# Kernel tuning notes

Hardware: AMD Instinct MI355X
Metric: run time of the kernel (lower is better)

Reference implementation:

```python
import jax, jax.numpy as jnp
import numpy as np

B, N, P = 64, 800000, 128          # batch, total CpG features, n_pathways (capsules)
H1, H2, C = 256, 128, 32           # MLP hidden_topology and n_output
EPS = 1e-5                         # BatchNorm1d eps


def _xavier(key, fan_in, fan_out, shape):
    bound = np.sqrt(6.0 / (fan_in + fan_out))
    return jax.random.uniform(key, shape, jnp.float32, -bound, bound)


def setup_inputs() -> dict:
    key = jax.random.key(0)
    ks = jax.random.split(key, 10)
    x = jax.random.normal(ks[0], (B, N), jnp.float32)
    # idx: sorted pathway assignment, equal capsule sizes N//P (matches module_lens)
    idx = jnp.sort(jax.random.randint(ks[1], (N,), 0, P)).astype(jnp.int64)
    # SPWModulesLayer.weight: xavier_uniform on shape (1, N)
    w = _xavier(ks[2], N, 1, (N,))
    co_w = jax.random.uniform(ks[3], (P,), jnp.float32, 0.0, 4.0)  # CancelOut init
    bn0_g, bn0_b = jnp.ones(P, jnp.float32), jnp.zeros(P, jnp.float32)
    W1, b1 = _xavier(ks[4], P, H1, (P, H1)), jnp.zeros(H1, jnp.float32)
    bn1_g, bn1_b = jnp.ones(H1, jnp.float32), jnp.zeros(H1, jnp.float32)
    W2, b2 = _xavier(ks[5], H1, H2, (H1, H2)), jnp.zeros(H2, jnp.float32)
    bn2_g, bn2_b = jnp.ones(H2, jnp.float32), jnp.zeros(H2, jnp.float32)
    Wo, bo = _xavier(ks[6], H2, C, (H2, C)), jnp.zeros(C, jnp.float32)
    return {"x": x, "w": w, "co_w": co_w,
            "bn0_g": bn0_g, "bn0_b": bn0_b,
            "W1": W1, "b1": b1, "bn1_g": bn1_g, "bn1_b": bn1_b,
            "W2": W2, "b2": b2, "bn2_g": bn2_g, "bn2_b": bn2_b,
            "Wo": Wo, "bo": bo, "idx": idx}


def _bn(z, g, b):
    # BatchNorm1d in training mode: batch mean, biased variance
    m = jnp.mean(z, axis=0)
    v = jnp.mean((z - m) ** 2, axis=0)
    return (z - m) * jax.lax.rsqrt(v + EPS) * g + b


def reference(x, w, co_w, bn0_g, bn0_b, W1, b1, bn1_g, bn1_b,
              W2, b2, bn2_g, bn2_b, Wo, bo, idx):
    # --- SPWModulesLayer: weighted scatter_add over pathway index (last dim) ---
    WX = jnp.zeros((x.shape[0], P), x.dtype).at[:, idx].add(x * w)   # [B, P]
    Z = _bn(jax.nn.relu(WX), bn0_g, bn0_b)                           # ReLU + BN
    Z = Z * jax.nn.sigmoid(co_w)                                     # CancelOut
    # --- MLP head: Linear->ReLU->BN twice, then Linear->Softmax ---
    h = _bn(jax.nn.relu(Z @ W1 + b1), bn1_g, bn1_b)
    h = _bn(jax.nn.relu(h @ W2 + b2), bn2_g, bn2_b)
    y = jax.nn.softmax(h @ Wo + bo, axis=-1)
    return (y, Z)
```

## Files before the change

kernel.cpp:

```cpp
#include <hip/hip_runtime.h>
#include <hip/hip_bf16.h>

#define BB     64
#define NF4    200000
#define NSEG   782
#define NP     128
#define NH1    256
#define NH2    128
#define NC     32
#define EPSV   1e-5f

typedef float fx4 __attribute__((ext_vector_type(4)));

__device__ __forceinline__ float dot4(fx4 a, fx4 b) {
    return fmaf(a[0], b[0], fmaf(a[1], b[1], fmaf(a[2], b[2], a[3] * b[3])));
}

__global__ __launch_bounds__(256) void k_scatter(
    const float* __restrict__ x, const float* __restrict__ w,
    const int* __restrict__ idx, float* __restrict__ WX)
{
    const int blk = blockIdx.x;
    const int b   = blk & 31;
    const int seg = blk >> 5;
    const int tid = threadIdx.x;
    const int n4  = seg * 256 + tid;
    const int waveBase = seg * 256 + (tid & ~63);
    if (waveBase + 63 >= NF4) {
        if (waveBase >= NF4) return;
    }
    if (n4 >= NF4) return;
    const int lane = tid & 63;

    const int  pLo = idx[waveBase * 4];
    const int  pHi = idx[waveBase * 4 + 255];
    const bool uniform = (pLo == pHi);

    const fx4  wv = reinterpret_cast<const fx4*>(w)[n4];
    const int4 pv = reinterpret_cast<const int4*>(idx)[n4];
    const fx4  xA = reinterpret_cast<const fx4*>(x)[(size_t)b * NF4 + n4];
    const fx4  xB = reinterpret_cast<const fx4*>(x)[(size_t)(b + 32) * NF4 + n4];

    fx4 wLo;
    wLo[0] = (pv.x == pLo) ? wv[0] : 0.f;
    wLo[1] = (pv.y == pLo) ? wv[1] : 0.f;
    wLo[2] = (pv.z == pLo) ? wv[2] : 0.f;
    wLo[3] = (pv.w == pLo) ? wv[3] : 0.f;

    float aLo = dot4(xA, wLo);
    float bLo = dot4(xB, wLo);
    #pragma unroll
    for (int off = 1; off < 64; off <<= 1) {
        aLo += __shfl_xor(aLo, off);
        bLo += __shfl_xor(bLo, off);
    }

    if (uniform) {
        const float val = (lane == 0) ? aLo : bLo;
        const int   row = (lane == 0) ? b : (b + 32);
        if (lane < 2)
            atomicAdd(&WX[row * NP + pLo], val);
    } else {
        fx4 wHi;
        wHi[0] = (pv.x == pHi) ? wv[0] : 0.f;
        wHi[1] = (pv.y == pHi) ? wv[1] : 0.f;
        wHi[2] = (pv.z == pHi) ? wv[2] : 0.f;
        wHi[3] = (pv.w == pHi) ? wv[3] : 0.f;
        float aHi = dot4(xA, wHi);
        float bHi = dot4(xB, wHi);
        #pragma unroll
        for (int off = 1; off < 64; off <<= 1) {
            aHi += __shfl_xor(aHi, off);
            bHi += __shfl_xor(bHi, off);
        }
        const float val = (lane == 0) ? aLo : ((lane == 1) ? bLo
                        : ((lane == 2) ? aHi : bHi));
        const int   row = ((lane & 1) == 0) ? b : (b + 32);
        const int   col = (lane < 2) ? pLo : pHi;
        if (lane < 4)
            atomicAdd(&WX[row * NP + col], val);
    }
}

__global__ void k_zero(float* __restrict__ WX)
{
    const int i = blockIdx.x * 256 + threadIdx.x;
    if (i < BB * NP) WX[i] = 0.f;
}

__device__ __forceinline__ float bn_shfl(float a, float gj, float bj)
{
    float s = a, q = a * a;
    #pragma unroll
    for (int off = 32; off > 0; off >>= 1) {
        s += __shfl_xor(s, off);
        q += __shfl_xor(q, off);
    }
    const float m   = s * (1.f / BB);
    const float var = q * (1.f / BB) - m * m;
    return (a - m) * rsqrtf(var + EPSV) * gj + bj;
}

__global__ __launch_bounds__(256) void k_fc1z(
    const float* __restrict__ WX,   const float* __restrict__ co_w,
    const float* __restrict__ bn0g, const float* __restrict__ bn0b,
    const float* __restrict__ W1,   const float* __restrict__ b1,
    const float* __restrict__ bn1g, const float* __restrict__ bn1b,
    float* __restrict__ Zout, float* __restrict__ h1t)
{
    __shared__ float Zl[NP * 65];
    const int tid  = threadIdx.x;
    const int wv   = tid >> 6;
    const int lane = tid & 63;
    const int blk  = blockIdx.x;

    if (tid < NP) {
        const int p = tid;
        float sum = 0.f, sq = 0.f;
        #pragma unroll 8
        for (int b = 0; b < BB; ++b) {
            const float r = fmaxf(WX[b * NP + p], 0.f);
            sum += r; sq += r * r;
        }
        const float m   = sum * (1.f / BB);
        const float var = sq * (1.f / BB) - m * m;
        const float sc  = rsqrtf(var + EPSV) * bn0g[p];
        const float bt  = bn0b[p];
        const float sig = 1.f / (1.f + expf(-co_w[p]));
        #pragma unroll 8
        for (int b = 0; b < BB; ++b) {
            const float r = fmaxf(WX[b * NP + p], 0.f);
            const float z = ((r - m) * sc + bt) * sig;
            Zl[p * 65 + b] = z;
            if (blk == 0) Zout[b * NP + p] = z;
        }
    }
    __syncthreads();

    const int j = blk * 4 + wv;
    float acc = b1[j];
    #pragma unroll 8
    for (int k = 0; k < NP; ++k)
        acc = fmaf(Zl[k * 65 + lane], W1[k * NH1 + j], acc);
    h1t[j * BB + lane] = bn_shfl(fmaxf(acc, 0.f), bn1g[j], bn1b[j]);
}

template <int K, int NOUT>
__global__ void k_fc_bn_t(const float* __restrict__ in_t,
                          const float* __restrict__ W,
                          const float* __restrict__ bias,
                          const float* __restrict__ g,
                          const float* __restrict__ beta,
                          float* __restrict__ out_t)
{
    const int j = blockIdx.x;
    const int b = threadIdx.x;
    float acc = bias[j];
    #pragma unroll 8
    for (int k = 0; k < K; ++k)
        acc = fmaf(in_t[k * BB + b], W[k * NOUT + j], acc);
    out_t[j * BB + b] = bn_shfl(fmaxf(acc, 0.f), g[j], beta[j]);
}

__global__ void k_head(const float* __restrict__ h2t,
                       const float* __restrict__ Wo,
                       const float* __restrict__ bo,
                       float* __restrict__ y)
{
    const int b = blockIdx.x;
    const int c = threadIdx.x;
    float acc = bo[c];
    #pragma unroll 8
    for (int k = 0; k < NH2; ++k)
        acc = fmaf(h2t[k * BB + b], Wo[k * NC + c], acc);
    float mx = acc;
    #pragma unroll
    for (int off = 16; off > 0; off >>= 1)
        mx = fmaxf(mx, __shfl_xor(mx, off));
    const float e = expf(acc - mx);
    float s = e;
    #pragma unroll
    for (int off = 16; off > 0; off >>= 1)
        s += __shfl_xor(s, off);
    y[b * NC + c] = e / s;
}

extern "C" void kernel_launch(void* const* d_in, const int* in_sizes, int n_in,
                              void* d_out, int out_size, void* d_ws, size_t ws_size,
                              hipStream_t stream)
{
    const float* x    = (const float*)d_in[0];
    const float* w    = (const float*)d_in[1];
    const float* co_w = (const float*)d_in[2];
    const float* bn0g = (const float*)d_in[3];
    const float* bn0b = (const float*)d_in[4];
    const float* W1   = (const float*)d_in[5];
    const float* b1   = (const float*)d_in[6];
    const float* bn1g = (const float*)d_in[7];
    const float* bn1b = (const float*)d_in[8];
    const float* W2   = (const float*)d_in[9];
    const float* b2   = (const float*)d_in[10];
    const float* bn2g = (const float*)d_in[11];
    const float* bn2b = (const float*)d_in[12];
    const float* Wo   = (const float*)d_in[13];
    const float* bo   = (const float*)d_in[14];
    const int*   idx  = (const int*)d_in[15];

    float* out = (float*)d_out;
    float* y   = out;
    float* Z   = out + BB * NC;

    float* WX  = (float*)d_ws;
    float* h1t = WX + BB * NP;
    float* h2t = h1t + BB * NH1;

    k_zero<<<32, 256, 0, stream>>>(WX);
    k_scatter<<<NSEG * 32, 256, 0, stream>>>(x, w, idx, WX);
    k_fc1z<<<64, 256, 0, stream>>>(WX, co_w, bn0g, bn0b,
                                   W1, b1, bn1g, bn1b, Z, h1t);
    k_fc_bn_t<NH1, NH2><<<NH2, BB, 0, stream>>>(h1t, W2, b2, bn2g, bn2b, h2t);
    k_head<<<BB, NC, 0, stream>>>(h2t, Wo, bo, y);
}
```

Before: 91.29 us.

## Split scatter into per-quad partial-dot stream pass plus segmented reduction kernel

```diff
diff --git a/kernel.cpp b/kernel.cpp
--- a/kernel.cpp
+++ b/kernel.cpp
@@ -3,12 +3,12 @@
 
 #define BB     64
 #define NF4    200000
-#define NSEG   782
 #define NP     128
 #define NH1    256
 #define NH2    128
 #define NC     32
 #define EPSV   1e-5f
+#define QTR    50000
 
 typedef float fx4 __attribute__((ext_vector_type(4)));
 
@@ -16,69 +16,81 @@
     return fmaf(a[0], b[0], fmaf(a[1], b[1], fmaf(a[2], b[2], a[3] * b[3])));
 }
 
-__global__ __launch_bounds__(256) void k_scatter(
+__global__ __launch_bounds__(256) void k_stream(
     const float* __restrict__ x, const float* __restrict__ w,
-    const int* __restrict__ idx, float* __restrict__ WX)
-{
-    const int blk = blockIdx.x;
-    const int b   = blk & 31;
-    const int seg = blk >> 5;
-    const int tid = threadIdx.x;
-    const int n4  = seg * 256 + tid;
-    const int waveBase = seg * 256 + (tid & ~63);
-    if (waveBase + 63 >= NF4) {
-        if (waveBase >= NF4) return;
-    }
+    const int* __restrict__ idx, float* __restrict__ y,
+    unsigned char* __restrict__ pq, float* __restrict__ WX)
+{
+    const int n4 = blockIdx.x * 256 + threadIdx.x;
     if (n4 >= NF4) return;
-    const int lane = tid & 63;
-
-    const int  pLo = idx[waveBase * 4];
-    const int  pHi = idx[waveBase * 4 + 255];
-    const bool uniform = (pLo == pHi);
+    const int b0 = blockIdx.y * 32;
 
     const fx4  wv = reinterpret_cast<const fx4*>(w)[n4];
     const int4 pv = reinterpret_cast<const int4*>(idx)[n4];
-    const fx4  xA = reinterpret_cast<const fx4*>(x)[(size_t)b * NF4 + n4];
-    const fx4  xB = reinterpret_cast<const fx4*>(x)[(size_t)(b + 32) * NF4 + n4];
-
-    fx4 wLo;
-    wLo[0] = (pv.x == pLo) ? wv[0] : 0.f;
-    wLo[1] = (pv.y == pLo) ? wv[1] : 0.f;
-    wLo[2] = (pv.z == pLo) ? wv[2] : 0.f;
-    wLo[3] = (pv.w == pLo) ? wv[3] : 0.f;
-
-    float aLo = dot4(xA, wLo);
-    float bLo = dot4(xB, wLo);
-    #pragma unroll
-    for (int off = 1; off < 64; off <<= 1) {
-        aLo += __shfl_xor(aLo, off);
-        bLo += __shfl_xor(bLo, off);
-    }
-
-    if (uniform) {
-        const float val = (lane == 0) ? aLo : bLo;
-        const int   row = (lane == 0) ? b : (b + 32);
-        if (lane < 2)
-            atomicAdd(&WX[row * NP + pLo], val);
+    if (blockIdx.y == 0) pq[n4] = (unsigned char)pv.x;
+
+    const fx4* __restrict__ xq = reinterpret_cast<const fx4*>(x);
+
+    if (pv.x == pv.w) {
+        #pragma unroll 8
+        for (int b = 0; b < 32; ++b)
+            y[(size_t)(b0 + b) * NF4 + n4] =
+                dot4(xq[(size_t)(b0 + b) * NF4 + n4], wv);
     } else {
-        fx4 wHi;
-        wHi[0] = (pv.x == pHi) ? wv[0] : 0.f;
-        wHi[1] = (pv.y == pHi) ? wv[1] : 0.f;
-        wHi[2] = (pv.z == pHi) ? wv[2] : 0.f;
-        wHi[3] = (pv.w == pHi) ? wv[3] : 0.f;
-        float aHi = dot4(xA, wHi);
-        float bHi = dot4(xB, wHi);
-        #pragma unroll
-        for (int off = 1; off < 64; off <<= 1) {
-            aHi += __shfl_xor(aHi, off);
-            bHi += __shfl_xor(bHi, off);
-        }
-        const float val = (lane == 0) ? aLo : ((lane == 1) ? bLo
-                        : ((lane == 2) ? aHi : bHi));
-        const int   row = ((lane & 1) == 0) ? b : (b + 32);
-        const int   col = (lane < 2) ? pLo : pHi;
-        if (lane < 4)
-            atomicAdd(&WX[row * NP + col], val);
+        fx4 wLo, wHi;
+        wLo[0] = wv[0];                         wHi[0] = (pv.x == pv.w) ? wv[0] : 0.f;
+        wLo[1] = (pv.y == pv.x) ? wv[1] : 0.f;  wHi[1] = (pv.y == pv.w) ? wv[1] : 0.f;
+        wLo[2] = (pv.z == pv.x) ? wv[2] : 0.f;  wHi[2] = (pv.z == pv.w) ? wv[2] : 0.f;
+        wLo[3] = (pv.w == pv.x) ? wv[3] : 0.f;  wHi[3] = wv[3];
+        for (int b = 0; b < 32; ++b) {
+            const fx4 xv = xq[(size_t)(b0 + b) * NF4 + n4];
+            y[(size_t)(b0 + b) * NF4 + n4] = dot4(xv, wLo);
+            atomicAdd(&WX[(b0 + b) * NP + pv.w], dot4(xv, wHi));
+        }
+    }
+}
+
+__global__ __launch_bounds__(256) void k_seg(
+    const float* __restrict__ y, const unsigned char* __restrict__ pq,
+    float* __restrict__ WX)
+{
+    __shared__ float lwx[NP];
+    const int b   = blockIdx.x >> 2;
+    const int s   = blockIdx.x & 3;
+    const int tid = threadIdx.x;
+    if (tid < NP) lwx[tid] = 0.f;
+    __syncthreads();
+
+    const fx4*   __restrict__ yq  = reinterpret_cast<const fx4*>(
+                                        y + (size_t)b * NF4 + s * QTR);
+    const uchar4* __restrict__ pqq = reinterpret_cast<const uchar4*>(pq + s * QTR);
+
+    float acc = 0.f;
+    int   curp = -1;
+    for (int i = tid; i < QTR / 4; i += 256) {
+        const fx4    v  = yq[i];
+        const uchar4 pz = pqq[i];
+        if (pz.x == pz.w) {
+            const float sv = (v[0] + v[1]) + (v[2] + v[3]);
+            if ((int)pz.x == curp) {
+                acc += sv;
+            } else {
+                if (curp >= 0) atomicAdd(&lwx[curp], acc);
+                curp = pz.x; acc = sv;
+            }
+        } else {
+            if (curp >= 0) { atomicAdd(&lwx[curp], acc); curp = -1; acc = 0.f; }
+            atomicAdd(&lwx[pz.x], v[0]);
+            atomicAdd(&lwx[pz.y], v[1]);
+            atomicAdd(&lwx[pz.z], v[2]);
+            atomicAdd(&lwx[pz.w], v[3]);
+        }
+    }
+    if (curp >= 0) atomicAdd(&lwx[curp], acc);
+    __syncthreads();
+    if (tid < NP) {
+        const float v = lwx[tid];
+        if (v != 0.f) atomicAdd(&WX[b * NP + tid], v);
     }
 }
 
@@ -207,17 +219,21 @@
     const int*   idx  = (const int*)d_in[15];
 
     float* out = (float*)d_out;
-    float* y   = out;
+    float* yo  = out;
     float* Z   = out + BB * NC;
 
     float* WX  = (float*)d_ws;
     float* h1t = WX + BB * NP;
     float* h2t = h1t + BB * NH1;
+    float* y   = h2t + BB * NH2;
+    unsigned char* pq = (unsigned char*)(y + (size_t)BB * NF4);
 
     k_zero<<<32, 256, 0, stream>>>(WX);
-    k_scatter<<<NSEG * 32, 256, 0, stream>>>(x, w, idx, WX);
+    dim3 sgrid((NF4 + 255) / 256, 2);
+    k_stream<<<sgrid, 256, 0, stream>>>(x, w, idx, y, pq, WX);
+    k_seg<<<BB * 4, 256, 0, stream>>>(y, pq, WX);
     k_fc1z<<<64, 256, 0, stream>>>(WX, co_w, bn0g, bn0b,
                                    W1, b1, bn1g, bn1b, Z, h1t);
     k_fc_bn_t<NH1, NH2><<<NH2, BB, 0, stream>>>(h1t, W2, b2, bn2g, bn2b, h2t);
-    k_head<<<BB, NC, 0, stream>>>(h2t, Wo, bo, y);
-}
+    k_head<<<BB, NC, 0, stream>>>(h2t, Wo, bo, yo);
+}
```

New measurement: 113.9 us. 1.25x slower.
